# Kernel tuning notes

Hardware: AMD Instinct MI355X
Metric: run time of the kernel (lower is better)

The kernel has to match this reference:

```python
import jax, jax.numpy as jnp
import numpy as np

ALPHA = 0.01  # leakyrelu negative slope


def setup_inputs() -> dict:
    key = jax.random.key(0)
    k1, k2, k3 = jax.random.split(key, 3)
    B, N, F_in, F_out = 32, 1024, 256, 256
    inp = jax.random.normal(k1, (B, N, F_in), dtype=jnp.float32)
    # xavier_uniform-like scale, gain=1.414
    lim_W = 1.414 * np.sqrt(6.0 / (F_in + F_out))
    W = jax.random.uniform(k2, (F_in, F_out), dtype=jnp.float32, minval=-lim_W, maxval=lim_W)
    lim_a = 1.414 * np.sqrt(6.0 / (2 * F_out + 1))
    a = jax.random.uniform(k3, (2 * F_out, 1), dtype=jnp.float32, minval=-lim_a, maxval=lim_a)
    return {"inp": inp, "W": W, "a": a}


def reference(inp, W, a):
    # h: [B, N, F_out]
    h = jnp.matmul(inp, W)
    F_out = W.shape[1]
    # Additive attention: score[b,i,j] = leakyrelu(h[b,i]@a1 + h[b,j]@a2).
    # Mathematically identical to cat([h_i, h_j]) @ a without materializing
    # the O(N^2 * 2F) a_input tensor.
    a1 = a[:F_out, 0]  # [F_out]
    a2 = a[F_out:, 0]  # [F_out]
    f1 = jnp.einsum('bnf,f->bn', h, a1)  # [B, N]
    f2 = jnp.einsum('bnf,f->bn', h, a2)  # [B, N]
    e = f1[:, :, None] + f2[:, None, :]  # [B, N, N]
    e = jnp.where(e > 0, e, ALPHA * e)   # leakyrelu
    attention = jax.nn.softmax(e, axis=-1)
    # dropout omitted (deterministic eval-mode reference)
    h_prime = jnp.matmul(attention, h)   # [B, N, F_out]
    return jax.nn.elu(h_prime)
```

## Files before the change

### kernel.cpp

```cpp
#include <hip/hip_runtime.h>
#include <hip/hip_bf16.h>

typedef unsigned short u16;
typedef unsigned int u32;
typedef __attribute__((ext_vector_type(4))) float f32x4;
typedef __attribute__((ext_vector_type(8))) short s16x8;
typedef __attribute__((ext_vector_type(4))) unsigned short u16x4;
typedef __attribute__((ext_vector_type(8))) unsigned short u16x8;

#define LRELU(x) ((x) > 0.f ? (x) : 0.01f * (x))

static __device__ __forceinline__ u16 f2bf(float x) {
    u32 u = __float_as_uint(x);
    return (u16)((u + 0x7fffu + ((u >> 16) & 1u)) >> 16);
}
static __device__ __forceinline__ float bf2f(u16 h) { return __uint_as_float((u32)h << 16); }

__global__ void k_prep(const float* __restrict__ W, const float* __restrict__ a,
                       u16* __restrict__ Wt_hi, u16* __restrict__ Wt_lo,
                       float* __restrict__ w1, float* __restrict__ w2) {
    int i = blockIdx.x, t = threadIdx.x;
    float x = W[i * 256 + t];
    float p1 = x * a[t];
    float p2 = x * a[256 + t];
#pragma unroll
    for (int off = 1; off < 64; off <<= 1) {
        p1 += __shfl_xor(p1, off);
        p2 += __shfl_xor(p2, off);
    }
    __shared__ float s1[4], s2[4];
    if ((t & 63) == 0) { s1[t >> 6] = p1; s2[t >> 6] = p2; }
    __syncthreads();
    if (t == 0) {
        w1[i] = s1[0] + s1[1] + s1[2] + s1[3];
        w2[i] = s2[0] + s2[1] + s2[2] + s2[3];
    }
    float y = W[t * 256 + i];
    u16 hi = f2bf(y);
    Wt_hi[i * 256 + t] = hi;
    Wt_lo[i * 256 + t] = f2bf(y - bf2f(hi));
}

__global__ void k_f(const float* __restrict__ inp, const float* __restrict__ w1,
                    const float* __restrict__ w2, float* __restrict__ f1,
                    float* __restrict__ f2) {
    __shared__ float sw1[256], sw2[256];
    int t = threadIdx.x;
    sw1[t] = w1[t];
    sw2[t] = w2[t];
    __syncthreads();
    int wv = t >> 6, l = t & 63;
    f32x4 c1 = *(const f32x4*)&sw1[l * 4];
    f32x4 c2 = *(const f32x4*)&sw2[l * 4];
    for (int it = 0; it < 16; ++it) {
        int row = blockIdx.x * 64 + wv * 16 + it;
        f32x4 v = *(const f32x4*)&inp[row * 256 + l * 4];
        float d1 = v.x * c1.x + v.y * c1.y + v.z * c1.z + v.w * c1.w;
        float d2 = v.x * c2.x + v.y * c2.y + v.z * c2.z + v.w * c2.w;
#pragma unroll
        for (int off = 1; off < 64; off <<= 1) {
            d1 += __shfl_xor(d1, off);
            d2 += __shfl_xor(d2, off);
        }
        if (l == 0) { f1[row] = d1; f2[row] = d2; }
    }
}

__global__ void k_m(const float* __restrict__ f2, float* __restrict__ Mb) {
    int b = blockIdx.x, t = threadIdx.x;
    float m = -1e30f;
#pragma unroll
    for (int j = 0; j < 4; ++j) m = fmaxf(m, f2[b * 1024 + t + j * 256]);
#pragma unroll
    for (int off = 1; off < 64; off <<= 1) m = fmaxf(m, __shfl_xor(m, off));
    __shared__ float s[4];
    if ((t & 63) == 0) s[t >> 6] = m;
    __syncthreads();
    if (t == 0) Mb[b] = fmaxf(fmaxf(s[0], s[1]), fmaxf(s[2], s[3]));
}

__global__ __launch_bounds__(256, 2) void k_h(const float* __restrict__ inp,
                                              const u16* __restrict__ Wt_hi,
                                              const u16* __restrict__ Wt_lo,
                                              u16* __restrict__ ht_hi,
                                              u16* __restrict__ ht_lo) {
    int t = threadIdx.x, w = t >> 6, l = t & 63, lr = l & 15, lk = l >> 4;
    int blkf = blockIdx.x >> 7;
    int blkn = blockIdx.x & 127;
    int f0 = blkf * 64;
    int n0 = blkn * 256;

    f32x4 acc[4][4];
#pragma unroll
    for (int i = 0; i < 4; ++i)
#pragma unroll
        for (int j = 0; j < 4; ++j)
#pragma unroll
            for (int r = 0; r < 4; ++r) acc[i][j][r] = 0.f;

    for (int kt = 0; kt < 8; ++kt) {
        int k0 = kt * 32 + lk * 8;
        s16x8 ah[4], al[4];
#pragma unroll
        for (int it = 0; it < 4; ++it) {
            int f = f0 + it * 16 + lr;
            ah[it] = *(const s16x8*)&Wt_hi[f * 256 + k0];
            al[it] = *(const s16x8*)&Wt_lo[f * 256 + k0];
        }
        s16x8 bh[4], bl[4];
#pragma unroll
        for (int ci = 0; ci < 4; ++ci) {
            int n = n0 + w * 64 + ci * 16 + lr;
            f32x4 v0 = *(const f32x4*)&inp[n * 256 + k0];
            f32x4 v1 = *(const f32x4*)&inp[n * 256 + k0 + 4];
            u16x8 hv, lv;
#pragma unroll
            for (int j = 0; j < 4; ++j) {
                u16 h0 = f2bf(v0[j]);
                hv[j] = h0;
                lv[j] = f2bf(v0[j] - bf2f(h0));
                u16 h1 = f2bf(v1[j]);
                hv[j + 4] = h1;
                lv[j + 4] = f2bf(v1[j] - bf2f(h1));
            }
            bh[ci] = *(s16x8*)&hv;
            bl[ci] = *(s16x8*)&lv;
        }
#pragma unroll
        for (int it = 0; it < 4; ++it)
#pragma unroll
            for (int ci = 0; ci < 4; ++ci) {
                acc[it][ci] = __builtin_amdgcn_mfma_f32_16x16x32_bf16(ah[it], bh[ci], acc[it][ci], 0, 0, 0);
                acc[it][ci] = __builtin_amdgcn_mfma_f32_16x16x32_bf16(ah[it], bl[ci], acc[it][ci], 0, 0, 0);
                acc[it][ci] = __builtin_amdgcn_mfma_f32_16x16x32_bf16(al[it], bh[ci], acc[it][ci], 0, 0, 0);
            }
    }
    int bb = n0 >> 10, nb0 = n0 & 1023;
#pragma unroll
    for (int it = 0; it < 4; ++it)
#pragma unroll
        for (int ci = 0; ci < 4; ++ci) {
            int col = nb0 + w * 64 + ci * 16 + lr;
#pragma unroll
            for (int r = 0; r < 4; ++r) {
                int F = f0 + it * 16 + lk * 4 + r;
                float x = acc[it][ci][r];
                u16 hh = f2bf(x);
                size_t o = (size_t)(bb * 256 + F) * 1024 + col;
                ht_hi[o] = hh;
                ht_lo[o] = f2bf(x - bf2f(hh));
            }
        }
}

__global__ __launch_bounds__(256, 2) void k_attn(const u16* __restrict__ ht_hi,
                                                 const u16* __restrict__ ht_lo,
                                                 const float* __restrict__ f1,
                                                 const float* __restrict__ f2,
                                                 const float* __restrict__ Mb,
                                                 float* __restrict__ out) {
    __shared__ float sf2[1024];
    __shared__ u16 P[2][4][4][512];
    __shared__ float rs[64];
    int t = threadIdx.x, w = t >> 6, l = t & 63, lr = l & 15, lk = l >> 4;
    int g = blockIdx.x;
    int xcd = g & 7, idx = g >> 3;
    int b = xcd * 4 + (idx >> 4);
    int i0 = (idx & 15) * 64;

    *(f32x4*)&sf2[t * 4] = *(const f32x4*)&f2[b * 1024 + t * 4];
    float Mv = Mb[b];
    int rowP = i0 + w * 16 + lr;
    float f1v = f1[b * 1024 + rowP];
    float miv = LRELU(f1v + Mv);
    float lsum = 0.f;
    const u16* Hh = ht_hi + (size_t)b * 256 * 1024;
    const u16* Hl = ht_lo + (size_t)b * 256 * 1024;

    auto computeP = [&](int cc2, int buf2) {
#pragma unroll
        for (int s = 0; s < 4; ++s) {
            int jb = cc2 * 128 + s * 32 + lk * 8;
            f32x4 fa = *(const f32x4*)&sf2[jb];
            f32x4 fb = *(const f32x4*)&sf2[jb + 4];
            u16x8 pv;
#pragma unroll
            for (int jj = 0; jj < 8; ++jj) {
                float fv = (jj < 4) ? fa[jj] : fb[jj - 4];
                float e = LRELU(f1v + fv);
                float p = __expf(e - miv);
                lsum += p;
                pv[jj] = f2bf(p);
            }
            *(u16x8*)&P[buf2][w][s][l * 8] = pv;
        }
    };

    f32x4 acc[4][4];
#pragma unroll
    for (int i = 0; i < 4; ++i)
#pragma unroll
        for (int j = 0; j < 4; ++j)
#pragma unroll
            for (int r = 0; r < 4; ++r) acc[i][j][r] = 0.f;

    __syncthreads();
    computeP(0, 0);

    for (int cc = 0; cc < 8; ++cc) {
        __syncthreads();
        if (cc < 7) computeP(cc + 1, (cc + 1) & 1);
        int buf = cc & 1;
#pragma unroll
        for (int s = 0; s < 4; ++s) {
            int jcol = cc * 128 + s * 32 + lk * 8;
            s16x8 pf[4];
#pragma unroll
            for (int it = 0; it < 4; ++it) pf[it] = *(const s16x8*)&P[buf][it][s][l * 8];
#pragma unroll
            for (int ci = 0; ci < 4; ++ci) {
                int f = w * 64 + ci * 16 + lr;
                s16x8 bh = *(const s16x8*)&Hh[(size_t)f * 1024 + jcol];
                s16x8 bl = *(const s16x8*)&Hl[(size_t)f * 1024 + jcol];
#pragma unroll
                for (int it = 0; it < 4; ++it) {
                    acc[it][ci] = __builtin_amdgcn_mfma_f32_16x16x32_bf16(pf[it], bh, acc[it][ci], 0, 0, 0);
                    acc[it][ci] = __builtin_amdgcn_mfma_f32_16x16x32_bf16(pf[it], bl, acc[it][ci], 0, 0, 0);
                }
            }
        }
    }

    lsum += __shfl_xor(lsum, 16);
    lsum += __shfl_xor(lsum, 32);
    if (l < 16) rs[w * 16 + lr] = lsum;
    __syncthreads();

#pragma unroll
    for (int it = 0; it < 4; ++it) {
        f32x4 sums = *(const f32x4*)&rs[it * 16 + lk * 4];
#pragma unroll
        for (int ci = 0; ci < 4; ++ci) {
            int col = w * 64 + ci * 16 + lr;
            int rowg = b * 1024 + i0 + it * 16 + lk * 4;
#pragma unroll
            for (int r = 0; r < 4; ++r) {
                float v = acc[it][ci][r] / sums[r];
                v = v > 0.f ? v : (__expf(v) - 1.f);
                out[(size_t)(rowg + r) * 256 + col] = v;
            }
        }
    }
}

extern "C" void kernel_launch(void* const* d_in, const int* in_sizes, int n_in,
                              void* d_out, int out_size, void* d_ws, size_t ws_size,
                              hipStream_t stream) {
    const float* inp = (const float*)d_in[0];
    const float* W = (const float*)d_in[1];
    const float* a = (const float*)d_in[2];
    float* out = (float*)d_out;

    char* ws = (char*)d_ws;
    u16* ht_hi = (u16*)(ws + 0);
    u16* ht_lo = (u16*)(ws + 16777216);
    u16* Wt_hi = (u16*)(ws + 33554432);
    u16* Wt_lo = (u16*)(ws + 33685504);
    float* w1 = (float*)(ws + 33816576);
    float* w2 = (float*)(ws + 33817600);
    float* f1 = (float*)(ws + 33818624);
    float* f2 = (float*)(ws + 33949696);
    float* Mb = (float*)(ws + 34080768);

    k_prep<<<256, 256, 0, stream>>>(W, a, Wt_hi, Wt_lo, w1, w2);
    k_f<<<512, 256, 0, stream>>>(inp, w1, w2, f1, f2);
    k_m<<<32, 256, 0, stream>>>(f2, Mb);
    k_h<<<512, 256, 0, stream>>>(inp, Wt_hi, Wt_lo, ht_hi, ht_lo);
    k_attn<<<512, 256, 0, stream>>>(ht_hi, ht_lo, f1, f2, Mb, out);
}
```

Measured before the change: 204.1 us.

## Retile h GEMM per row block and split attention rows across eight waves

The k_h GEMM now gives each block 64 node rows across all 256 output features, one 64-feature slice per wave. The input rows are therefore read and split into hi/lo bf16 once per block instead of once per feature block. The attention kernel grows to 512 threads. Each wave handles half the row groups for its feature slice and half of the P tiles, so accumulator registers shrink and more waves can hide latency. MFMA sections are also wrapped in raised wave priority. The trade-off is that each H fragment now feeds only two row groups instead of four, which doubles H loads per block, and row sums now need a cross-wave combine.

```diff
diff --git a/kernel.cpp b/kernel.cpp
--- a/kernel.cpp
+++ b/kernel.cpp
@@ -85,10 +85,8 @@
                                               u16* __restrict__ ht_hi,
                                               u16* __restrict__ ht_lo) {
     int t = threadIdx.x, w = t >> 6, l = t & 63, lr = l & 15, lk = l >> 4;
-    int blkf = blockIdx.x >> 7;
-    int blkn = blockIdx.x & 127;
-    int f0 = blkf * 64;
-    int n0 = blkn * 256;
+    int n0 = blockIdx.x * 64;
+    int bb = n0 >> 10, nb0 = n0 & 1023;
 
     f32x4 acc[4][4];
 #pragma unroll
@@ -103,14 +101,14 @@
         s16x8 ah[4], al[4];
 #pragma unroll
         for (int it = 0; it < 4; ++it) {
-            int f = f0 + it * 16 + lr;
+            int f = w * 64 + it * 16 + lr;
             ah[it] = *(const s16x8*)&Wt_hi[f * 256 + k0];
             al[it] = *(const s16x8*)&Wt_lo[f * 256 + k0];
         }
         s16x8 bh[4], bl[4];
 #pragma unroll
         for (int ci = 0; ci < 4; ++ci) {
-            int n = n0 + w * 64 + ci * 16 + lr;
+            int n = n0 + ci * 16 + lr;
             f32x4 v0 = *(const f32x4*)&inp[n * 256 + k0];
             f32x4 v1 = *(const f32x4*)&inp[n * 256 + k0 + 4];
             u16x8 hv, lv;
@@ -135,15 +133,14 @@
                 acc[it][ci] = __builtin_amdgcn_mfma_f32_16x16x32_bf16(al[it], bh[ci], acc[it][ci], 0, 0, 0);
             }
     }
-    int bb = n0 >> 10, nb0 = n0 & 1023;
 #pragma unroll
     for (int it = 0; it < 4; ++it)
 #pragma unroll
         for (int ci = 0; ci < 4; ++ci) {
-            int col = nb0 + w * 64 + ci * 16 + lr;
+            int col = nb0 + ci * 16 + lr;
 #pragma unroll
             for (int r = 0; r < 4; ++r) {
-                int F = f0 + it * 16 + lk * 4 + r;
+                int F = w * 64 + it * 16 + lk * 4 + r;
                 float x = acc[it][ci][r];
                 u16 hh = f2bf(x);
                 size_t o = (size_t)(bb * 256 + F) * 1024 + col;
@@ -153,7 +150,7 @@
         }
 }
 
-__global__ __launch_bounds__(256, 2) void k_attn(const u16* __restrict__ ht_hi,
+__global__ __launch_bounds__(512, 4) void k_attn(const u16* __restrict__ ht_hi,
                                                  const u16* __restrict__ ht_lo,
                                                  const float* __restrict__ f1,
                                                  const float* __restrict__ f2,
@@ -161,25 +158,28 @@
                                                  float* __restrict__ out) {
     __shared__ float sf2[1024];
     __shared__ u16 P[2][4][4][512];
-    __shared__ float rs[64];
+    __shared__ float rs[128];
     int t = threadIdx.x, w = t >> 6, l = t & 63, lr = l & 15, lk = l >> 4;
+    int wf = w & 3, wr = w >> 2;
     int g = blockIdx.x;
     int xcd = g & 7, idx = g >> 3;
     int b = xcd * 4 + (idx >> 4);
     int i0 = (idx & 15) * 64;
 
-    *(f32x4*)&sf2[t * 4] = *(const f32x4*)&f2[b * 1024 + t * 4];
+    if (t < 256) *(f32x4*)&sf2[t * 4] = *(const f32x4*)&f2[b * 1024 + t * 4];
     float Mv = Mb[b];
-    int rowP = i0 + w * 16 + lr;
-    float f1v = f1[b * 1024 + rowP];
+    int rgp = wf;
+    int sh = wr;
+    float f1v = f1[b * 1024 + i0 + rgp * 16 + lr];
     float miv = LRELU(f1v + Mv);
     float lsum = 0.f;
-    const u16* Hh = ht_hi + (size_t)b * 256 * 1024;
-    const u16* Hl = ht_lo + (size_t)b * 256 * 1024;
+    const u16* Hh = ht_hi + (size_t)b * 262144;
+    const u16* Hl = ht_lo + (size_t)b * 262144;
 
     auto computeP = [&](int cc2, int buf2) {
 #pragma unroll
-        for (int s = 0; s < 4; ++s) {
+        for (int ss = 0; ss < 2; ++ss) {
+            int s = sh * 2 + ss;
             int jb = cc2 * 128 + s * 32 + lk * 8;
             f32x4 fa = *(const f32x4*)&sf2[jb];
             f32x4 fb = *(const f32x4*)&sf2[jb + 4];
@@ -192,13 +192,13 @@
                 lsum += p;
                 pv[jj] = f2bf(p);
             }
-            *(u16x8*)&P[buf2][w][s][l * 8] = pv;
+            *(u16x8*)&P[buf2][rgp][s][l * 8] = pv;
         }
     };
 
-    f32x4 acc[4][4];
-#pragma unroll
-    for (int i = 0; i < 4; ++i)
+    f32x4 acc[2][4];
+#pragma unroll
+    for (int i = 0; i < 2; ++i)
 #pragma unroll
         for (int j = 0; j < 4; ++j)
 #pragma unroll
@@ -214,19 +214,20 @@
 #pragma unroll
         for (int s = 0; s < 4; ++s) {
             int jcol = cc * 128 + s * 32 + lk * 8;
-            s16x8 pf[4];
-#pragma unroll
-            for (int it = 0; it < 4; ++it) pf[it] = *(const s16x8*)&P[buf][it][s][l * 8];
+            s16x8 pf[2];
+            pf[0] = *(const s16x8*)&P[buf][wr * 2][s][l * 8];
+            pf[1] = *(const s16x8*)&P[buf][wr * 2 + 1][s][l * 8];
 #pragma unroll
             for (int ci = 0; ci < 4; ++ci) {
-                int f = w * 64 + ci * 16 + lr;
+                int f = wf * 64 + ci * 16 + lr;
                 s16x8 bh = *(const s16x8*)&Hh[(size_t)f * 1024 + jcol];
                 s16x8 bl = *(const s16x8*)&Hl[(size_t)f * 1024 + jcol];
-#pragma unroll
-                for (int it = 0; it < 4; ++it) {
-                    acc[it][ci] = __builtin_amdgcn_mfma_f32_16x16x32_bf16(pf[it], bh, acc[it][ci], 0, 0, 0);
-                    acc[it][ci] = __builtin_amdgcn_mfma_f32_16x16x32_bf16(pf[it], bl, acc[it][ci], 0, 0, 0);
-                }
+                __builtin_amdgcn_s_setprio(1);
+                acc[0][ci] = __builtin_amdgcn_mfma_f32_16x16x32_bf16(pf[0], bh, acc[0][ci], 0, 0, 0);
+                acc[0][ci] = __builtin_amdgcn_mfma_f32_16x16x32_bf16(pf[0], bl, acc[0][ci], 0, 0, 0);
+                acc[1][ci] = __builtin_amdgcn_mfma_f32_16x16x32_bf16(pf[1], bh, acc[1][ci], 0, 0, 0);
+                acc[1][ci] = __builtin_amdgcn_mfma_f32_16x16x32_bf16(pf[1], bl, acc[1][ci], 0, 0, 0);
+                __builtin_amdgcn_s_setprio(0);
             }
         }
     }
@@ -237,12 +238,15 @@
     __syncthreads();
 
 #pragma unroll
-    for (int it = 0; it < 4; ++it) {
-        f32x4 sums = *(const f32x4*)&rs[it * 16 + lk * 4];
+    for (int it = 0; it < 2; ++it) {
+        int rg = wr * 2 + it;
+        f32x4 s1 = *(const f32x4*)&rs[rg * 16 + lk * 4];
+        f32x4 s2 = *(const f32x4*)&rs[(rg + 4) * 16 + lk * 4];
+        f32x4 sums = s1 + s2;
 #pragma unroll
         for (int ci = 0; ci < 4; ++ci) {
-            int col = w * 64 + ci * 16 + lr;
-            int rowg = b * 1024 + i0 + it * 16 + lk * 4;
+            int col = wf * 64 + ci * 16 + lr;
+            int rowg = b * 1024 + i0 + rg * 16 + lk * 4;
 #pragma unroll
             for (int r = 0; r < 4; ++r) {
                 float v = acc[it][ci][r] / sums[r];
@@ -276,5 +280,5 @@
     k_f<<<512, 256, 0, stream>>>(inp, w1, w2, f1, f2);
     k_m<<<32, 256, 0, stream>>>(f2, Mb);
     k_h<<<512, 256, 0, stream>>>(inp, Wt_hi, Wt_lo, ht_hi, ht_lo);
-    k_attn<<<512, 256, 0, stream>>>(ht_hi, ht_lo, f1, f2, Mb, out);
-}
+    k_attn<<<512, 512, 0, stream>>>(ht_hi, ht_lo, f1, f2, Mb, out);
+}
```

Result: slower. 250.4 us (+22.7%).
